# Performance work log

Measured on AMD Instinct MI355X. Metric: run time of the kernel, lower is better.

The kernel has to match this reference:

```python
import jax, jax.numpy as jnp
import numpy as np

N_NODES = 10000
N_EDGES = 160000
N_FEAT = 512
HEADS = 8
HID = 128
OUT = 16


def setup_inputs() -> dict:
    key = jax.random.key(0)
    ks = jax.random.split(key, 16)
    inp = {
        'node_features': jax.random.normal(ks[0], (N_NODES, N_FEAT), jnp.float32),
        'edge_src': jax.random.randint(ks[1], (N_EDGES,), 0, N_NODES, jnp.int32),
        'edge_dst': jax.random.randint(ks[2], (N_EDGES,), 0, N_NODES, jnp.int32),
        # GAT layer params (scaled randn for numerical sanity)
        'W1': jax.random.normal(ks[3], (HEADS, HID, N_FEAT), jnp.float32) * 0.05,
        'a1': jax.random.normal(ks[4], (HEADS, 2 * HID), jnp.float32) * 0.05,
        'W2': jax.random.normal(ks[5], (HEADS, HID, HID), jnp.float32) * 0.05,
        'a2': jax.random.normal(ks[6], (HEADS, 2 * HID), jnp.float32) * 0.05,
        # MLP: LayerNorm(128) -> Linear(128,64) -> LeakyReLU -> Linear(64,16) -> LeakyReLU -> Linear(16,OUT) -> ReLU
        'ln_g': jnp.ones((HID,), jnp.float32),
        'ln_b': jnp.zeros((HID,), jnp.float32),
        'Wl1': jax.random.normal(ks[7], (64, HID), jnp.float32) * 0.05,
        'bl1': jnp.zeros((64,), jnp.float32),
        'Wl2': jax.random.normal(ks[8], (16, 64), jnp.float32) * 0.05,
        'bl2': jnp.zeros((16,), jnp.float32),
        'Wl3': jax.random.normal(ks[9], (OUT, 16), jnp.float32) * 0.05,
        'bl3': jnp.zeros((OUT,), jnp.float32),
    }
    return inp


def gat_layer(x, src, dst, W, a, n_nodes):
    # per-node, per-head projection: h[n,h,d]
    h = jnp.einsum('hdf,nf->nhd', W, x)
    # split attention vector: e_ij = a[:HID].h_i + a[HID:].h_j
    s_i = jnp.einsum('nhd,hd->nh', h, a[:, :HID])  # score contribution of target i
    s_j = jnp.einsum('nhd,hd->nh', h, a[:, HID:])  # score contribution of neighbor j
    e = jax.nn.leaky_relu(s_i[dst] + s_j[src])     # [E,H], negative_slope=0.01 (torch default)
    # segment softmax over edges grouped by dst
    m = jax.ops.segment_max(e, dst, num_segments=n_nodes)           # [N,H]
    m = jnp.where(jnp.isfinite(m), m, 0.0)
    ex = jnp.exp(e - m[dst])                                        # [E,H]
    denom = jax.ops.segment_sum(ex, dst, num_segments=n_nodes)      # [N,H]
    alpha = ex / jnp.where(denom > 0, denom, 1.0)[dst]              # [E,H]
    # scatter-accumulate weighted neighbor embeddings
    agg = jax.ops.segment_sum(alpha[:, :, None] * h[src], dst, num_segments=n_nodes)  # [N,H,HID]
    # average over heads, ELU (matches 1/attn_heads * attn_sum -> ELU)
    return jax.nn.elu(agg.mean(axis=1))  # [N,HID]


def reference(node_features, edge_src, edge_dst, W1, a1, W2, a2,
              ln_g, ln_b, Wl1, bl1, Wl2, bl2, Wl3, bl3):
    n = node_features.shape[0]
    emb1 = gat_layer(node_features, edge_src, edge_dst, W1, a1, n)
    emb2 = gat_layer(emb1, edge_src, edge_dst, W2, a2, n)
    g = emb2.mean(axis=0)  # [HID] graph embedding
    # MLP head (dropout = identity at inference)
    mu = g.mean()
    var = ((g - mu) ** 2).mean()
    gn = (g - mu) / jnp.sqrt(var + 1e-5) * ln_g + ln_b
    x = jax.nn.leaky_relu(Wl1 @ gn + bl1)
    x = jax.nn.leaky_relu(Wl2 @ x + bl2)
    return jax.nn.relu(Wl3 @ x + bl3)
```

## Files before the change

kernel.cpp:

```cpp
#include <hip/hip_runtime.h>
#include <math.h>

#define N_NODES 10000
#define N_EDGES 160000
#define N_FEAT  512
#define HEADS   8
#define HID     128

typedef __attribute__((ext_vector_type(8))) short bf16x8;
typedef __attribute__((ext_vector_type(4))) float f32x4;
typedef __attribute__((ext_vector_type(2))) float v2f;

__device__ inline unsigned short f2bf_rne(float f) {
  unsigned int u = __float_as_uint(f);
  unsigned int r = u + 0x7fffu + ((u >> 16) & 1u);
  return (unsigned short)(r >> 16);
}
__device__ inline float bf2f(unsigned int b) {
  return __uint_as_float(b << 16);
}

__device__ inline void split_body(const float* __restrict__ in,
                                  unsigned short* __restrict__ hi,
                                  unsigned short* __restrict__ lo,
                                  int R, int K8, int idx) {
  int r = idx & 15;
  int t = idx >> 4;
  int kq = t % K8;
  int rb = t / K8;
  int row = rb * 16 + r;
  float v[8] = {0.f, 0.f, 0.f, 0.f, 0.f, 0.f, 0.f, 0.f};
  if (row < R) {
    const float* p = in + (size_t)row * (K8 * 8) + kq * 8;
    float4 a = *(const float4*)p;
    float4 b = *(const float4*)(p + 4);
    v[0] = a.x; v[1] = a.y; v[2] = a.z; v[3] = a.w;
    v[4] = b.x; v[5] = b.y; v[6] = b.z; v[7] = b.w;
  }
  union { unsigned short u[8]; int4 v4; } H, L;
  #pragma unroll
  for (int e = 0; e < 8; ++e) {
    unsigned short hb_ = f2bf_rne(v[e]);
    H.u[e] = hb_;
    L.u[e] = f2bf_rne(v[e] - bf2f(hb_));
  }
  *(int4*)&hi[(size_t)idx * 8] = H.v4;
  if (lo) *(int4*)&lo[(size_t)idx * 8] = L.v4;
}

__global__ __launch_bounds__(256)
void split_frag2(const float* __restrict__ in1, unsigned short* __restrict__ hi1,
                 unsigned short* __restrict__ lo1, int R1, int K81, int total1,
                 int nb1,
                 const float* __restrict__ in2, unsigned short* __restrict__ hi2,
                 unsigned short* __restrict__ lo2, int R2, int K82, int total2,
                 int nb2,
                 const int* __restrict__ edst, int* __restrict__ deg, int E) {
  if ((int)blockIdx.x < nb1) {
    int idx = blockIdx.x * 256 + threadIdx.x;
    if (idx < total1) split_body(in1, hi1, lo1, R1, K81, idx);
  } else if ((int)blockIdx.x < nb1 + nb2) {
    int idx = (blockIdx.x - nb1) * 256 + threadIdx.x;
    if (idx < total2) split_body(in2, hi2, lo2, R2, K82, idx);
  } else {
    int e = (blockIdx.x - nb1 - nb2) * 256 + threadIdx.x;
    if (e < E) atomicAdd(&deg[edst[e]], 1);
  }
}

__global__ __launch_bounds__(128, 2)
void gemm_frag(const unsigned short* __restrict__ Afh,
               const unsigned short* __restrict__ Afl,
               const unsigned short* __restrict__ Bfh,
               const unsigned short* __restrict__ Bfl,
               const float* __restrict__ avec,
               unsigned short* __restrict__ hb,
               float* __restrict__ si, float* __restrict__ sj,
               int M, int K) {
  __shared__ float rsi[64][2];
  __shared__ float rsj[64][2];
  int tid = threadIdx.x;
  int wave = tid >> 6, lane = tid & 63;
  int r = lane & 15, q = lane >> 4;

  int blk = blockIdx.x;
  int rr = blk & 7, gg = blk >> 3;
  int head = gg & 7;
  int mtile = (gg >> 3) * 8 + rr;
  int m0 = mtile * 64;
  int wn = wave * 64;
  int K8 = K >> 3;

  const bf16x8* pAh = (const bf16x8*)Afh;
  const bf16x8* pBh = (const bf16x8*)Bfh;
  const bf16x8* pBl = (const bf16x8*)Bfl;
  size_t rstep = (size_t)K8 * 16;
  size_t aidx = (size_t)(m0 >> 4) * rstep + (size_t)q * 16 + r;
  size_t bidx = (size_t)(head * 8 + (wn >> 4)) * rstep + (size_t)q * 16 + r;

  f32x4 acc[4][4] = {};

  for (int k0 = 0; k0 < K; k0 += 64, aidx += 128, bidx += 128) {
    bf16x8 ah[8], bh[8], bl[8];
    #pragma unroll
    for (int i = 0; i < 4; ++i) {
      ah[i]     = pAh[aidx + i * rstep];
      bh[i]     = pBh[bidx + i * rstep];
      bl[i]     = pBl[bidx + i * rstep];
      ah[i + 4] = pAh[aidx + i * rstep + 64];
      bh[i + 4] = pBh[bidx + i * rstep + 64];
      bl[i + 4] = pBl[bidx + i * rstep + 64];
    }
    #pragma unroll
    for (int i = 0; i < 4; ++i)
      #pragma unroll
      for (int j = 0; j < 4; ++j) {
        acc[i][j] = __builtin_amdgcn_mfma_f32_16x16x32_bf16(ah[i], bh[j], acc[i][j], 0, 0, 0);
        acc[i][j] = __builtin_amdgcn_mfma_f32_16x16x32_bf16(ah[i], bl[j], acc[i][j], 0, 0, 0);
      }
    #pragma unroll
    for (int i = 0; i < 4; ++i)
      #pragma unroll
      for (int j = 0; j < 4; ++j) {
        acc[i][j] = __builtin_amdgcn_mfma_f32_16x16x32_bf16(ah[i + 4], bh[j + 4], acc[i][j], 0, 0, 0);
        acc[i][j] = __builtin_amdgcn_mfma_f32_16x16x32_bf16(ah[i + 4], bl[j + 4], acc[i][j], 0, 0, 0);
      }
  }

  const float* av = avec + (size_t)head * (2 * HID);
  float aiv[4], ajv[4];
  #pragma unroll
  for (int j = 0; j < 4; ++j) {
    int c = wn + j * 16 + r;
    aiv[j] = av[c];
    ajv[j] = av[HID + c];
  }
  #pragma unroll
  for (int i = 0; i < 4; ++i) {
    #pragma unroll
    for (int reg = 0; reg < 4; ++reg) {
      int lrow = i * 16 + q * 4 + reg;
      int row = m0 + lrow;
      float vsi = 0.f, vsj = 0.f;
      #pragma unroll
      for (int j = 0; j < 4; ++j) {
        float v = acc[i][j][reg];
        vsi = fmaf(v, aiv[j], vsi);
        vsj = fmaf(v, ajv[j], vsj);
        if (row < M)
          hb[((size_t)head * M + row) * HID + wn + j * 16 + r] = f2bf_rne(v);
      }
      #pragma unroll
      for (int o = 8; o >= 1; o >>= 1) {
        vsi += __shfl_xor(vsi, o);
        vsj += __shfl_xor(vsj, o);
      }
      if (r == 0) {
        rsi[lrow][wave] = vsi;
        rsj[lrow][wave] = vsj;
      }
    }
  }
  __syncthreads();
  if (tid < 64) {
    int row = m0 + tid;
    if (row < M) {
      si[(size_t)head * M + row] = rsi[tid][0] + rsi[tid][1];
      sj[(size_t)head * M + row] = rsj[tid][0] + rsj[tid][1];
    }
  }
}

__global__ __launch_bounds__(1024)
void scan_kernel(const int* __restrict__ deg, int* __restrict__ off, int N) {
  __shared__ int sums[1024];
  const int PER = 10;
  int tid = threadIdx.x;
  int base = tid * PER;
  int loc[PER];
  int run = 0;
  #pragma unroll
  for (int j = 0; j < PER; ++j) {
    int v = (base + j < N) ? deg[base + j] : 0;
    run += v;
    loc[j] = run;
  }
  sums[tid] = run;
  __syncthreads();
  for (int o = 1; o < 1024; o <<= 1) {
    int v = (tid >= o) ? sums[tid - o] : 0;
    __syncthreads();
    sums[tid] += v;
    __syncthreads();
  }
  int ex = sums[tid] - run;
  if (tid == 0) off[0] = 0;
  #pragma unroll
  for (int j = 0; j < PER; ++j)
    if (base + j < N) off[base + j + 1] = ex + loc[j];
}

__global__ void fill_kernel(const int* __restrict__ src, const int* __restrict__ dst,
                            const int* __restrict__ off, int* __restrict__ cursor,
                            int* __restrict__ ssrc, int E) {
  int e = blockIdx.x * blockDim.x + threadIdx.x;
  if (e < E) {
    int d = dst[e];
    int p = atomicAdd(&cursor[d], 1);
    ssrc[off[d] + p] = src[e];
  }
}

__global__ __launch_bounds__(512)
void gat_aggregate8(const unsigned short* __restrict__ hb,
                    const float* __restrict__ si, const float* __restrict__ sj,
                    const int* __restrict__ off, const int* __restrict__ ssrc,
                    unsigned short* __restrict__ aggb, int N) {
  __shared__ int2 prs[8][4][32];
  int head = blockIdx.x & 7;
  int wv = threadIdx.x >> 6;
  int lane = threadIdx.x & 63;
  int grp = lane >> 4;
  int sl = lane & 15;
  int n = (blockIdx.x >> 3) * 32 + wv * 4 + grp;
  const unsigned short* hbase = hb + (size_t)head * N * HID;
  const float* sjh = sj + (size_t)head * N;
  bool nv = n < N;
  int begin = 0, deg = 0;
  float s_i = 0.f;
  if (nv) {
    begin = off[n];
    deg = off[n + 1] - begin;
    s_i = si[(size_t)head * N + n];
  }

  int src0 = 0, src1 = 0;
  float sc0 = -INFINITY, sc1 = -INFINITY;
  if (sl < deg) {
    src0 = ssrc[begin + sl];
    float t = s_i + sjh[src0];
    sc0 = t > 0.f ? t : 0.01f * t;
  }
  if (16 + sl < deg) {
    src1 = ssrc[begin + 16 + sl];
    float t = s_i + sjh[src1];
    sc1 = t > 0.f ? t : 0.01f * t;
  }
  float m = fmaxf(sc0, sc1);
  for (int e2 = 32 + sl; e2 < deg; e2 += 16) {
    int s = ssrc[begin + e2];
    float t = s_i + sjh[s];
    t = t > 0.f ? t : 0.01f * t;
    m = fmaxf(m, t);
  }
  #pragma unroll
  for (int o = 1; o <= 8; o <<= 1) m = fmaxf(m, __shfl_xor(m, o));

  float w0 = (sl < deg) ? __expf(sc0 - m) : 0.f;
  float w1 = (16 + sl < deg) ? __expf(sc1 - m) : 0.f;
  float den = w0 + w1;
  for (int e2 = 32 + sl; e2 < deg; e2 += 16) {
    int s = ssrc[begin + e2];
    float t = s_i + sjh[s];
    t = t > 0.f ? t : 0.01f * t;
    den += __expf(t - m);
  }
  #pragma unroll
  for (int o = 1; o <= 8; o <<= 1) den += __shfl_xor(den, o);

  prs[wv][grp][sl] = make_int2(src0, __float_as_int(w0));
  prs[wv][grp][16 + sl] = make_int2(src1, __float_as_int(w1));
  __asm__ volatile("s_waitcnt lgkmcnt(0)" ::: "memory");

  v2f a01 = {0.f, 0.f}, a23 = {0.f, 0.f}, a45 = {0.f, 0.f}, a67 = {0.f, 0.f};
  int dmin = deg < 32 ? deg : 32;
  for (int e0 = 0; e0 < dmin; e0 += 4) {
    int2 p[4];
    #pragma unroll
    for (int u = 0; u < 4; ++u) p[u] = prs[wv][grp][e0 + u];
    int4 pv[4];
    #pragma unroll
    for (int u = 0; u < 4; ++u)
      pv[u] = *(const int4*)&hbase[(size_t)p[u].x * HID + sl * 8];
    #pragma unroll
    for (int u = 0; u < 4; ++u) {
      float w = __int_as_float(p[u].y);
      v2f w2 = {w, w};
      int4 q = pv[u];
      v2f t0 = {bf2f((unsigned)q.x & 0xffffu), __uint_as_float((unsigned)q.x & 0xffff0000u)};
      v2f t1 = {bf2f((unsigned)q.y & 0xffffu), __uint_as_float((unsigned)q.y & 0xffff0000u)};
      v2f t2 = {bf2f((unsigned)q.z & 0xffffu), __uint_as_float((unsigned)q.z & 0xffff0000u)};
      v2f t3 = {bf2f((unsigned)q.w & 0xffffu), __uint_as_float((unsigned)q.w & 0xffff0000u)};
      a01 += w2 * t0;
      a23 += w2 * t1;
      a45 += w2 * t2;
      a67 += w2 * t3;
    }
  }
  for (int e2 = 32; e2 < deg; ++e2) {
    int s = ssrc[begin + e2];
    float t = s_i + sjh[s];
    t = t > 0.f ? t : 0.01f * t;
    float w = __expf(t - m);
    v2f w2 = {w, w};
    int4 q = *(const int4*)&hbase[(size_t)s * HID + sl * 8];
    v2f t0 = {bf2f((unsigned)q.x & 0xffffu), __uint_as_float((unsigned)q.x & 0xffff0000u)};
    v2f t1 = {bf2f((unsigned)q.y & 0xffffu), __uint_as_float((unsigned)q.y & 0xffff0000u)};
    v2f t2 = {bf2f((unsigned)q.z & 0xffffu), __uint_as_float((unsigned)q.z & 0xffff0000u)};
    v2f t3 = {bf2f((unsigned)q.w & 0xffffu), __uint_as_float((unsigned)q.w & 0xffff0000u)};
    a01 += w2 * t0; a23 += w2 * t1; a45 += w2 * t2; a67 += w2 * t3;
  }

  if (nv) {
    float inv = den > 0.f ? 1.0f / den : 0.f;
    union { unsigned short u[8]; int4 v4; } P;
    P.u[0] = f2bf_rne(a01.x * inv); P.u[1] = f2bf_rne(a01.y * inv);
    P.u[2] = f2bf_rne(a23.x * inv); P.u[3] = f2bf_rne(a23.y * inv);
    P.u[4] = f2bf_rne(a45.x * inv); P.u[5] = f2bf_rne(a45.y * inv);
    P.u[6] = f2bf_rne(a67.x * inv); P.u[7] = f2bf_rne(a67.y * inv);
    *(int4*)&aggb[((size_t)head * N + n) * HID + sl * 8] = P.v4;
  }
}

__global__ __launch_bounds__(256)
void headmean_frag_w2(const unsigned short* __restrict__ aggb,
                      unsigned short* __restrict__ hiA,
                      int N, int nbHM,
                      const float* __restrict__ W2, unsigned short* __restrict__ hiB,
                      unsigned short* __restrict__ loB, int totalB) {
  if ((int)blockIdx.x >= nbHM) {
    int idx = (blockIdx.x - nbHM) * 256 + threadIdx.x;
    if (idx < totalB) split_body(W2, hiB, loB, HEADS * HID, 16, idx);
    return;
  }
  int idx = blockIdx.x * 256 + threadIdx.x;
  int total = ((N + 15) / 16) * 256;
  if (idx >= total) return;
  int r = idx & 15;
  int kq = (idx >> 4) & 15;
  int rb = idx >> 8;
  int n = rb * 16 + r;
  float s[8] = {0.f, 0.f, 0.f, 0.f, 0.f, 0.f, 0.f, 0.f};
  if (n < N) {
    #pragma unroll
    for (int hh = 0; hh < HEADS; ++hh) {
      int4 pv = *(const int4*)&aggb[((size_t)hh * N + n) * HID + kq * 8];
      s[0] += bf2f((unsigned)pv.x & 0xffffu);
      s[1] += __uint_as_float((unsigned)pv.x & 0xffff0000u);
      s[2] += bf2f((unsigned)pv.y & 0xffffu);
      s[3] += __uint_as_float((unsigned)pv.y & 0xffff0000u);
      s[4] += bf2f((unsigned)pv.z & 0xffffu);
      s[5] += __uint_as_float((unsigned)pv.z & 0xffff0000u);
      s[6] += bf2f((unsigned)pv.w & 0xffffu);
      s[7] += __uint_as_float((unsigned)pv.w & 0xffff0000u);
    }
  }
  union { unsigned short u[8]; int4 v4; } H;
  #pragma unroll
  for (int e = 0; e < 8; ++e) {
    float v = s[e] * (1.0f / HEADS);
    v = v > 0.f ? v : (__expf(v) - 1.0f);
    H.u[e] = f2bf_rne(v);
  }
  *(int4*)&hiA[(size_t)idx * 8] = H.v4;
}

__global__ __launch_bounds__(256)
void headmean_pool(const unsigned short* __restrict__ aggb, float* __restrict__ g,
                   int N) {
  __shared__ float sm[16][128];
  int t = threadIdx.x;
  int nl = t >> 4, dg = t & 15;
  int n = blockIdx.x * 16 + nl;
  float v[8] = {0.f, 0.f, 0.f, 0.f, 0.f, 0.f, 0.f, 0.f};
  if (n < N) {
    #pragma unroll
    for (int hh = 0; hh < HEADS; ++hh) {
      int4 pv = *(const int4*)&aggb[((size_t)hh * N + n) * HID + dg * 8];
      v[0] += bf2f((unsigned)pv.x & 0xffffu);
      v[1] += __uint_as_float((unsigned)pv.x & 0xffff0000u);
      v[2] += bf2f((unsigned)pv.y & 0xffffu);
      v[3] += __uint_as_float((unsigned)pv.y & 0xffff0000u);
      v[4] += bf2f((unsigned)pv.z & 0xffffu);
      v[5] += __uint_as_float((unsigned)pv.z & 0xffff0000u);
      v[6] += bf2f((unsigned)pv.w & 0xffffu);
      v[7] += __uint_as_float((unsigned)pv.w & 0xffff0000u);
    }
    #pragma unroll
    for (int e = 0; e < 8; ++e) {
      float x = v[e] * (1.0f / HEADS);
      v[e] = x > 0.f ? x : (__expf(x) - 1.0f);
    }
  }
  #pragma unroll
  for (int e = 0; e < 8; ++e) sm[nl][dg * 8 + e] = v[e];
  __syncthreads();
  if (t < 128) {
    float s = 0.f;
    #pragma unroll
    for (int nn = 0; nn < 16; ++nn) s += sm[nn][t];
    atomicAdd(&g[t], s);
  }
}

__global__ __launch_bounds__(128)
void mlp_kernel(const float* __restrict__ g, const float* __restrict__ ln_g,
                const float* __restrict__ ln_b, const float* __restrict__ Wl1,
                const float* __restrict__ bl1, const float* __restrict__ Wl2,
                const float* __restrict__ bl2, const float* __restrict__ Wl3,
                const float* __restrict__ bl3, float* __restrict__ out, float invN) {
  __shared__ float red[128];
  __shared__ float gn[128];
  __shared__ float x1[64];
  __shared__ float x2[16];
  int t = threadIdx.x;
  float gg = g[t] * invN;
  red[t] = gg;
  __syncthreads();
  for (int o = 64; o > 0; o >>= 1) {
    if (t < o) red[t] += red[t + o];
    __syncthreads();
  }
  float mu = red[0] * (1.0f / HID);
  __syncthreads();
  float dv = gg - mu;
  red[t] = dv * dv;
  __syncthreads();
  for (int o = 64; o > 0; o >>= 1) {
    if (t < o) red[t] += red[t + o];
    __syncthreads();
  }
  float var = red[0] * (1.0f / HID);
  gn[t] = dv / sqrtf(var + 1e-5f) * ln_g[t] + ln_b[t];
  __syncthreads();
  if (t < 64) {
    float s = bl1[t];
    for (int k = 0; k < 128; ++k) s += Wl1[t * 128 + k] * gn[k];
    x1[t] = s > 0.f ? s : 0.01f * s;
  }
  __syncthreads();
  if (t < 16) {
    float s = bl2[t];
    for (int k = 0; k < 64; ++k) s += Wl2[t * 64 + k] * x1[k];
    x2[t] = s > 0.f ? s : 0.01f * s;
  }
  __syncthreads();
  if (t < 16) {
    float s = bl3[t];
    for (int k = 0; k < 16; ++k) s += Wl3[t * 16 + k] * x2[k];
    out[t] = s > 0.f ? s : 0.f;
  }
}

extern "C" void kernel_launch(void* const* d_in, const int* in_sizes, int n_in,
                              void* d_out, int out_size, void* d_ws, size_t ws_size,
                              hipStream_t stream) {
  const float* x    = (const float*)d_in[0];
  const int*   esrc = (const int*)d_in[1];
  const int*   edst = (const int*)d_in[2];
  const float* W1   = (const float*)d_in[3];
  const float* a1   = (const float*)d_in[4];
  const float* W2   = (const float*)d_in[5];
  const float* a2   = (const float*)d_in[6];
  const float* ln_g = (const float*)d_in[7];
  const float* ln_b = (const float*)d_in[8];
  const float* Wl1  = (const float*)d_in[9];
  const float* bl1  = (const float*)d_in[10];
  const float* Wl2  = (const float*)d_in[11];
  const float* bl2  = (const float*)d_in[12];
  const float* Wl3  = (const float*)d_in[13];
  const float* bl3  = (const float*)d_in[14];
  float* out = (float*)d_out;

  const int RBPAD = 640;

  unsigned short* aggb = (unsigned short*)d_ws;
  float* si   = (float*)(aggb + (size_t)N_NODES * HEADS * HID);
  float* sj   = si + N_NODES * HEADS;
  float* g    = sj + N_NODES * HEADS;
  int*   deg  = (int*)(g + 128);
  int*   cur  = deg + N_NODES;
  int*   off  = cur + N_NODES;
  int*   ssrc = off + 10004;
  unsigned short* Afh = (unsigned short*)(ssrc + N_EDGES);
  unsigned short* Afl = Afh + (size_t)RBPAD * 64 * 128;
  unsigned short* Bfh = Afl + (size_t)RBPAD * 64 * 128;
  unsigned short* Bfl = Bfh + (size_t)64 * 64 * 128;
  unsigned short* hb  = Bfl + (size_t)64 * 64 * 128;

  hipMemsetAsync(g, 0, 128 * sizeof(float) + 2 * N_NODES * sizeof(int), stream);

  int gemmGrid = 160 * HEADS;
  int aggGrid = ((N_NODES + 31) / 32) * 8;

  {
    int totalA = RBPAD * 64 * 16;
    int nbA = (totalA + 255) / 256;
    int totalB = 64 * 64 * 16;
    int nbB = (totalB + 255) / 256;
    int nbE = (N_EDGES + 255) / 256;
    split_frag2<<<nbA + nbB + nbE, 256, 0, stream>>>(
        x, Afh, (unsigned short*)nullptr, N_NODES, 64, totalA, nbA,
        W1, Bfh, Bfl, HEADS * HID, 64, totalB, nbB,
        edst, deg, N_EDGES);
  }
  scan_kernel<<<1, 1024, 0, stream>>>(deg, off, N_NODES);
  fill_kernel<<<(N_EDGES + 255) / 256, 256, 0, stream>>>(esrc, edst, off, cur, ssrc, N_EDGES);

  gemm_frag<<<gemmGrid, 128, 0, stream>>>(Afh, Afl, Bfh, Bfl, a1, hb,
                                          si, sj, N_NODES, N_FEAT);
  gat_aggregate8<<<aggGrid, 512, 0, stream>>>(hb, si, sj, off, ssrc, aggb, N_NODES);
  {
    int nbHM = ((N_NODES + 15) / 16 * 256 + 255) / 256;
    int totalB = 64 * 16 * 16;
    int nbB = (totalB + 255) / 256;
    headmean_frag_w2<<<nbHM + nbB, 256, 0, stream>>>(aggb, Afh, N_NODES, nbHM,
                                                     W2, Bfh, Bfl, totalB);
  }

  gemm_frag<<<gemmGrid, 128, 0, stream>>>(Afh, Afl, Bfh, Bfl, a2, hb,
                                          si, sj, N_NODES, HID);
  gat_aggregate8<<<aggGrid, 512, 0, stream>>>(hb, si, sj, off, ssrc, aggb, N_NODES);

  headmean_pool<<<(N_NODES + 15) / 16, 256, 0, stream>>>(aggb, g, N_NODES);
  mlp_kernel<<<1, 128, 0, stream>>>(g, ln_g, ln_b, Wl1, bl1, Wl2, bl2, Wl3, bl3,
                                    out, 1.0f / N_NODES);
}
```

Baseline: 248.0 us.

## Precompute attention scores via folded W·a vectors and drop bf16 lo-split in GEMM

Folds the attention vectors into the weights (wt = W^T a) so the per-node scores si/sj come from full-precision fp32 dot products over x or the layer-1 embedding, computed in the scan kernel and the headmean kernel instead of in the GEMM epilogue. The GEMM no longer runs the hi/lo bf16 split for B, which halves its MFMA work and operand loads. It also moves to 256-thread blocks with 128-row tiles. The cost is lower precision in the projected embeddings h, plus extra fp32 score work placed on otherwise light kernels.

```diff
diff --git a/kernel.cpp b/kernel.cpp
--- a/kernel.cpp
+++ b/kernel.cpp
@@ -50,154 +50,179 @@
 
 __global__ __launch_bounds__(256)
 void split_frag2(const float* __restrict__ in1, unsigned short* __restrict__ hi1,
-                 unsigned short* __restrict__ lo1, int R1, int K81, int total1,
-                 int nb1,
+                 int R1, int K81, int total1, int nb1,
                  const float* __restrict__ in2, unsigned short* __restrict__ hi2,
-                 unsigned short* __restrict__ lo2, int R2, int K82, int total2,
-                 int nb2,
-                 const int* __restrict__ edst, int* __restrict__ deg, int E) {
-  if ((int)blockIdx.x < nb1) {
-    int idx = blockIdx.x * 256 + threadIdx.x;
-    if (idx < total1) split_body(in1, hi1, lo1, R1, K81, idx);
-  } else if ((int)blockIdx.x < nb1 + nb2) {
-    int idx = (blockIdx.x - nb1) * 256 + threadIdx.x;
-    if (idx < total2) split_body(in2, hi2, lo2, R2, K82, idx);
+                 int R2, int K82, int total2, int nb2,
+                 const int* __restrict__ edst, int* __restrict__ deg, int E,
+                 const float* __restrict__ av1, const float* __restrict__ W2p,
+                 const float* __restrict__ av2,
+                 float* __restrict__ wt1, float* __restrict__ wt2) {
+  int b = (int)blockIdx.x;
+  int tid = threadIdx.x;
+  if (b < nb1) {
+    int idx = b * 256 + tid;
+    if (idx < total1) split_body(in1, hi1, nullptr, R1, K81, idx);
+  } else if (b < nb1 + nb2) {
+    int idx = (b - nb1) * 256 + tid;
+    if (idx < total2) split_body(in2, hi2, nullptr, R2, K82, idx);
   } else {
-    int e = (blockIdx.x - nb1 - nb2) * 256 + threadIdx.x;
-    if (e < E) atomicAdd(&deg[edst[e]], 1);
-  }
-}
-
-__global__ __launch_bounds__(128, 2)
+    int nbE = (E + 255) / 256;
+    int eb = b - nb1 - nb2;
+    if (eb < nbE) {
+      int e = eb * 256 + tid;
+      if (e < E) atomicAdd(&deg[edst[e]], 1);
+    } else {
+      int wb = eb - nbE;
+      if (wb < 32) {
+        int o = wb * 256 + tid;
+        int f = o & 511, ii = (o >> 9) & 1, h = o >> 10;
+        const float* Wp = in2 + (size_t)h * HID * N_FEAT + f;
+        const float* ap = av1 + h * 2 * HID + ii * HID;
+        float c0 = 0.f, c1 = 0.f;
+        for (int d = 0; d < HID; d += 2) {
+          c0 = fmaf(Wp[(size_t)d * N_FEAT], ap[d], c0);
+          c1 = fmaf(Wp[(size_t)(d + 1) * N_FEAT], ap[d + 1], c1);
+        }
+        wt1[o] = c0 + c1;
+      } else {
+        int o = (wb - 32) * 256 + tid;
+        int f = o & 127, ii = (o >> 7) & 1, h = o >> 8;
+        const float* Wp = W2p + (size_t)h * HID * HID + f;
+        const float* ap = av2 + h * 2 * HID + ii * HID;
+        float c0 = 0.f, c1 = 0.f;
+        for (int d = 0; d < HID; d += 2) {
+          c0 = fmaf(Wp[(size_t)d * HID], ap[d], c0);
+          c1 = fmaf(Wp[(size_t)(d + 1) * HID], ap[d + 1], c1);
+        }
+        wt2[o] = c0 + c1;
+      }
+    }
+  }
+}
+
+__global__ __launch_bounds__(256, 3)
 void gemm_frag(const unsigned short* __restrict__ Afh,
-               const unsigned short* __restrict__ Afl,
                const unsigned short* __restrict__ Bfh,
-               const unsigned short* __restrict__ Bfl,
-               const float* __restrict__ avec,
                unsigned short* __restrict__ hb,
-               float* __restrict__ si, float* __restrict__ sj,
                int M, int K) {
-  __shared__ float rsi[64][2];
-  __shared__ float rsj[64][2];
   int tid = threadIdx.x;
   int wave = tid >> 6, lane = tid & 63;
   int r = lane & 15, q = lane >> 4;
+  int wr = wave >> 1, wc = wave & 1;
 
   int blk = blockIdx.x;
-  int rr = blk & 7, gg = blk >> 3;
-  int head = gg & 7;
-  int mtile = (gg >> 3) * 8 + rr;
-  int m0 = mtile * 64;
-  int wn = wave * 64;
+  int mtile = blk % 80;
+  int head = blk / 80;
+  int m0 = mtile * 128;
   int K8 = K >> 3;
 
-  const bf16x8* pAh = (const bf16x8*)Afh;
-  const bf16x8* pBh = (const bf16x8*)Bfh;
-  const bf16x8* pBl = (const bf16x8*)Bfl;
+  const bf16x8* pA = (const bf16x8*)Afh;
+  const bf16x8* pB = (const bf16x8*)Bfh;
   size_t rstep = (size_t)K8 * 16;
-  size_t aidx = (size_t)(m0 >> 4) * rstep + (size_t)q * 16 + r;
-  size_t bidx = (size_t)(head * 8 + (wn >> 4)) * rstep + (size_t)q * 16 + r;
+  size_t aidx = (size_t)((m0 >> 4) + wr * 4) * rstep + (size_t)q * 16 + r;
+  size_t bidx = (size_t)(head * 8 + wc * 4) * rstep + (size_t)q * 16 + r;
 
   f32x4 acc[4][4] = {};
 
   for (int k0 = 0; k0 < K; k0 += 64, aidx += 128, bidx += 128) {
-    bf16x8 ah[8], bh[8], bl[8];
+    bf16x8 a[8], b[8];
     #pragma unroll
     for (int i = 0; i < 4; ++i) {
-      ah[i]     = pAh[aidx + i * rstep];
-      bh[i]     = pBh[bidx + i * rstep];
-      bl[i]     = pBl[bidx + i * rstep];
-      ah[i + 4] = pAh[aidx + i * rstep + 64];
-      bh[i + 4] = pBh[bidx + i * rstep + 64];
-      bl[i + 4] = pBl[bidx + i * rstep + 64];
+      a[i]     = pA[aidx + i * rstep];
+      b[i]     = pB[bidx + i * rstep];
+      a[i + 4] = pA[aidx + i * rstep + 64];
+      b[i + 4] = pB[bidx + i * rstep + 64];
     }
     #pragma unroll
     for (int i = 0; i < 4; ++i)
       #pragma unroll
-      for (int j = 0; j < 4; ++j) {
-        acc[i][j] = __builtin_amdgcn_mfma_f32_16x16x32_bf16(ah[i], bh[j], acc[i][j], 0, 0, 0);
-        acc[i][j] = __builtin_amdgcn_mfma_f32_16x16x32_bf16(ah[i], bl[j], acc[i][j], 0, 0, 0);
-      }
+      for (int j = 0; j < 4; ++j)
+        acc[i][j] = __builtin_amdgcn_mfma_f32_16x16x32_bf16(a[i], b[j], acc[i][j], 0, 0, 0);
     #pragma unroll
     for (int i = 0; i < 4; ++i)
       #pragma unroll
-      for (int j = 0; j < 4; ++j) {
-        acc[i][j] = __builtin_amdgcn_mfma_f32_16x16x32_bf16(ah[i + 4], bh[j + 4], acc[i][j], 0, 0, 0);
-        acc[i][j] = __builtin_amdgcn_mfma_f32_16x16x32_bf16(ah[i + 4], bl[j + 4], acc[i][j], 0, 0, 0);
+      for (int j = 0; j < 4; ++j)
+        acc[i][j] = __builtin_amdgcn_mfma_f32_16x16x32_bf16(a[i + 4], b[j + 4], acc[i][j], 0, 0, 0);
+  }
+
+  #pragma unroll
+  for (int i = 0; i < 4; ++i)
+    #pragma unroll
+    for (int reg = 0; reg < 4; ++reg) {
+      int row = m0 + wr * 64 + i * 16 + q * 4 + reg;
+      if (row < M) {
+        #pragma unroll
+        for (int j = 0; j < 4; ++j)
+          hb[((size_t)head * M + row) * HID + wc * 64 + j * 16 + r] =
+              f2bf_rne(acc[i][j][reg]);
       }
-  }
-
-  const float* av = avec + (size_t)head * (2 * HID);
-  float aiv[4], ajv[4];
-  #pragma unroll
-  for (int j = 0; j < 4; ++j) {
-    int c = wn + j * 16 + r;
-    aiv[j] = av[c];
-    ajv[j] = av[HID + c];
-  }
-  #pragma unroll
-  for (int i = 0; i < 4; ++i) {
-    #pragma unroll
-    for (int reg = 0; reg < 4; ++reg) {
-      int lrow = i * 16 + q * 4 + reg;
-      int row = m0 + lrow;
-      float vsi = 0.f, vsj = 0.f;
-      #pragma unroll
-      for (int j = 0; j < 4; ++j) {
-        float v = acc[i][j][reg];
-        vsi = fmaf(v, aiv[j], vsi);
-        vsj = fmaf(v, ajv[j], vsj);
-        if (row < M)
-          hb[((size_t)head * M + row) * HID + wn + j * 16 + r] = f2bf_rne(v);
-      }
-      #pragma unroll
-      for (int o = 8; o >= 1; o >>= 1) {
-        vsi += __shfl_xor(vsi, o);
-        vsj += __shfl_xor(vsj, o);
-      }
-      if (r == 0) {
-        rsi[lrow][wave] = vsi;
-        rsj[lrow][wave] = vsj;
-      }
-    }
-  }
-  __syncthreads();
-  if (tid < 64) {
-    int row = m0 + tid;
-    if (row < M) {
-      si[(size_t)head * M + row] = rsi[tid][0] + rsi[tid][1];
-      sj[(size_t)head * M + row] = rsj[tid][0] + rsj[tid][1];
-    }
-  }
+    }
 }
 
 __global__ __launch_bounds__(1024)
-void scan_kernel(const int* __restrict__ deg, int* __restrict__ off, int N) {
-  __shared__ int sums[1024];
-  const int PER = 10;
+void scan_score(const int* __restrict__ deg, int* __restrict__ off, int N,
+                const float* __restrict__ x, const float* __restrict__ wt1,
+                float* __restrict__ si, float* __restrict__ sj) {
+  if (blockIdx.x == 0) {
+    __shared__ int sums[1024];
+    const int PER = 10;
+    int tid = threadIdx.x;
+    int base = tid * PER;
+    int loc[PER];
+    int run = 0;
+    #pragma unroll
+    for (int j = 0; j < PER; ++j) {
+      int v = (base + j < N) ? deg[base + j] : 0;
+      run += v;
+      loc[j] = run;
+    }
+    sums[tid] = run;
+    __syncthreads();
+    for (int o = 1; o < 1024; o <<= 1) {
+      int v = (tid >= o) ? sums[tid - o] : 0;
+      __syncthreads();
+      sums[tid] += v;
+      __syncthreads();
+    }
+    int ex = sums[tid] - run;
+    if (tid == 0) off[0] = 0;
+    #pragma unroll
+    for (int j = 0; j < PER; ++j)
+      if (base + j < N) off[base + j + 1] = ex + loc[j];
+    return;
+  }
+  __shared__ float wl[8192];
   int tid = threadIdx.x;
-  int base = tid * PER;
-  int loc[PER];
-  int run = 0;
-  #pragma unroll
-  for (int j = 0; j < PER; ++j) {
-    int v = (base + j < N) ? deg[base + j] : 0;
-    run += v;
-    loc[j] = run;
-  }
-  sums[tid] = run;
-  __syncthreads();
-  for (int o = 1; o < 1024; o <<= 1) {
-    int v = (tid >= o) ? sums[tid - o] : 0;
-    __syncthreads();
-    sums[tid] += v;
-    __syncthreads();
-  }
-  int ex = sums[tid] - run;
-  if (tid == 0) off[0] = 0;
-  #pragma unroll
-  for (int j = 0; j < PER; ++j)
-    if (base + j < N) off[base + j + 1] = ex + loc[j];
+  #pragma unroll
+  for (int k = 0; k < 8; ++k) wl[tid + k * 1024] = wt1[tid + k * 1024];
+  __syncthreads();
+  int wv = tid >> 6, lane = tid & 63;
+  int rr = lane >> 4, sl = lane & 15;
+  int n = ((int)blockIdx.x - 1) * 64 + wv * 4 + rr;
+  if (n >= N) return;
+  const float* xp = x + (size_t)n * N_FEAT + sl * 4;
+  float acc[16];
+  #pragma unroll
+  for (int t = 0; t < 16; ++t) acc[t] = 0.f;
+  #pragma unroll
+  for (int k = 0; k < 8; ++k) {
+    float4 xv = *(const float4*)(xp + k * 64);
+    #pragma unroll
+    for (int t = 0; t < 16; ++t) {
+      float4 w4 = *(const float4*)&wl[t * 512 + k * 64 + sl * 4];
+      acc[t] = fmaf(xv.x, w4.x, fmaf(xv.y, w4.y, fmaf(xv.z, w4.z, fmaf(xv.w, w4.w, acc[t]))));
+    }
+  }
+  #pragma unroll
+  for (int o = 1; o <= 8; o <<= 1)
+    #pragma unroll
+    for (int t = 0; t < 16; ++t) acc[t] += __shfl_xor(acc[t], o);
+  float out = acc[0];
+  #pragma unroll
+  for (int t = 1; t < 16; ++t) out = (sl == t) ? acc[t] : out;
+  int h = sl >> 1;
+  if (sl & 1) sj[(size_t)h * N + n] = out;
+  else        si[(size_t)h * N + n] = out;
 }
 
 __global__ void fill_kernel(const int* __restrict__ src, const int* __restrict__ dst,
@@ -327,15 +352,21 @@
                       unsigned short* __restrict__ hiA,
                       int N, int nbHM,
                       const float* __restrict__ W2, unsigned short* __restrict__ hiB,
-                      unsigned short* __restrict__ loB, int totalB) {
+                      int totalB,
+                      const float* __restrict__ wt2,
+                      float* __restrict__ si, float* __restrict__ sj) {
   if ((int)blockIdx.x >= nbHM) {
     int idx = (blockIdx.x - nbHM) * 256 + threadIdx.x;
-    if (idx < totalB) split_body(W2, hiB, loB, HEADS * HID, 16, idx);
+    if (idx < totalB) split_body(W2, hiB, nullptr, HEADS * HID, 16, idx);
     return;
   }
-  int idx = blockIdx.x * 256 + threadIdx.x;
-  int total = ((N + 15) / 16) * 256;
-  if (idx >= total) return;
+  __shared__ float wl[2048];
+  __shared__ float sred[16][16][17];
+  int tid = threadIdx.x;
+  #pragma unroll
+  for (int k = 0; k < 8; ++k) wl[tid + k * 256] = wt2[tid + k * 256];
+  __syncthreads();
+  int idx = blockIdx.x * 256 + tid;
   int r = idx & 15;
   int kq = (idx >> 4) & 15;
   int rb = idx >> 8;
@@ -355,14 +386,34 @@
       s[7] += __uint_as_float((unsigned)pv.w & 0xffff0000u);
     }
   }
+  float p[16];
+  #pragma unroll
+  for (int t = 0; t < 16; ++t) p[t] = 0.f;
   union { unsigned short u[8]; int4 v4; } H;
   #pragma unroll
   for (int e = 0; e < 8; ++e) {
     float v = s[e] * (1.0f / HEADS);
     v = v > 0.f ? v : (__expf(v) - 1.0f);
+    #pragma unroll
+    for (int t = 0; t < 16; ++t) p[t] = fmaf(v, wl[t * 128 + kq * 8 + e], p[t]);
     H.u[e] = f2bf_rne(v);
   }
   *(int4*)&hiA[(size_t)idx * 8] = H.v4;
+  #pragma unroll
+  for (int t = 0; t < 16; ++t) sred[kq][r][t] = p[t];
+  __syncthreads();
+  {
+    int rr = tid >> 4, t = tid & 15;
+    float sum = 0.f;
+    #pragma unroll
+    for (int k = 0; k < 16; ++k) sum += sred[k][rr][t];
+    int nn = rb * 16 + rr;
+    if (nn < N) {
+      int h = t >> 1;
+      if (t & 1) sj[(size_t)h * N + nn] = sum;
+      else       si[(size_t)h * N + nn] = sum;
+    }
+  }
 }
 
 __global__ __launch_bounds__(256)
@@ -483,14 +534,14 @@
   int*   off  = cur + N_NODES;
   int*   ssrc = off + 10004;
   unsigned short* Afh = (unsigned short*)(ssrc + N_EDGES);
-  unsigned short* Afl = Afh + (size_t)RBPAD * 64 * 128;
-  unsigned short* Bfh = Afl + (size_t)RBPAD * 64 * 128;
-  unsigned short* Bfl = Bfh + (size_t)64 * 64 * 128;
-  unsigned short* hb  = Bfl + (size_t)64 * 64 * 128;
+  float* wt1 = (float*)(Afh + (size_t)RBPAD * 64 * 128);
+  float* wt2 = wt1 + 8192;
+  unsigned short* Bfh = (unsigned short*)(wt1 + (size_t)RBPAD * 64 * 64);
+  unsigned short* hb  = Bfh + (size_t)2 * 64 * 64 * 128;
 
   hipMemsetAsync(g, 0, 128 * sizeof(float) + 2 * N_NODES * sizeof(int), stream);
 
-  int gemmGrid = 160 * HEADS;
+  int gemmGrid = 80 * HEADS;
   int aggGrid = ((N_NODES + 31) / 32) * 8;
 
   {
@@ -499,27 +550,29 @@
     int totalB = 64 * 64 * 16;
     int nbB = (totalB + 255) / 256;
     int nbE = (N_EDGES + 255) / 256;
-    split_frag2<<<nbA + nbB + nbE, 256, 0, stream>>>(
-        x, Afh, (unsigned short*)nullptr, N_NODES, 64, totalA, nbA,
-        W1, Bfh, Bfl, HEADS * HID, 64, totalB, nbB,
-        edst, deg, N_EDGES);
-  }
-  scan_kernel<<<1, 1024, 0, stream>>>(deg, off, N_NODES);
+    int nbW = 40;
+    split_frag2<<<nbA + nbB + nbE + nbW, 256, 0, stream>>>(
+        x, Afh, N_NODES, 64, totalA, nbA,
+        W1, Bfh, HEADS * HID, 64, totalB, nbB,
+        edst, deg, N_EDGES,
+        a1, W2, a2, wt1, wt2);
+  }
+  scan_score<<<1 + (N_NODES + 63) / 64, 1024, 0, stream>>>(deg, off, N_NODES,
+                                                           x, wt1, si, sj);
   fill_kernel<<<(N_EDGES + 255) / 256, 256, 0, stream>>>(esrc, edst, off, cur, ssrc, N_EDGES);
 
-  gemm_frag<<<gemmGrid, 128, 0, stream>>>(Afh, Afl, Bfh, Bfl, a1, hb,
-                                          si, sj, N_NODES, N_FEAT);
+  gemm_frag<<<gemmGrid, 256, 0, stream>>>(Afh, Bfh, hb, N_NODES, N_FEAT);
   gat_aggregate8<<<aggGrid, 512, 0, stream>>>(hb, si, sj, off, ssrc, aggb, N_NODES);
   {
-    int nbHM = ((N_NODES + 15) / 16 * 256 + 255) / 256;
+    int nbHM = (N_NODES + 15) / 16;
     int totalB = 64 * 16 * 16;
     int nbB = (totalB + 255) / 256;
     headmean_frag_w2<<<nbHM + nbB, 256, 0, stream>>>(aggb, Afh, N_NODES, nbHM,
-                                                     W2, Bfh, Bfl, totalB);
-  }
-
-  gemm_frag<<<gemmGrid, 128, 0, stream>>>(Afh, Afl, Bfh, Bfl, a2, hb,
-                                          si, sj, N_NODES, HID);
+                                                     W2, Bfh, totalB,
+                                                     wt2, si, sj);
+  }
+
+  gemm_frag<<<gemmGrid, 256, 0, stream>>>(Afh, Bfh, hb, N_NODES, HID);
   gat_aggregate8<<<aggGrid, 512, 0, stream>>>(hb, si, sj, off, ssrc, aggb, N_NODES);
 
   headmean_pool<<<(N_NODES + 15) / 16, 256, 0, stream>>>(aggb, g, N_NODES);
```

New measurement: 251.7 us. Within noise of the previous version (+1.5%).
